# Performance work log

Hardware: AMD Instinct MI355X
Metric: run time of the kernel (lower is better)

The kernel has to match this reference:

```python
import jax, jax.numpy as jnp
import numpy as np

T, B, D = 512, 256, 2048   # seq_len, batch, input_dim
Q = 1                      # n_qubits == hidden_dim (forced by measure Linear(n_wires,1) applied to [B,1])
G = 4                      # gates: forget, input, update, output


def setup_inputs() -> dict:
    key = jax.random.key(0)
    ks = jax.random.split(key, 8)
    s_lin = 1.0 / np.sqrt(D + Q)   # torch Linear default init bound
    s_q = 1.0 / np.sqrt(Q)
    u = lambda k, shape, s: jax.random.uniform(k, shape, jnp.float32, -s, s)
    return {
        "inputs": jax.random.normal(ks[0], (T, B, D), jnp.float32),
        # stacked per-gate params (gate order: forget, input, update, output)
        "linear_w": u(ks[1], (G, Q, D + Q), s_lin),
        "linear_b": u(ks[2], (G, Q), s_lin),
        "enc_w": u(ks[3], (G, Q, Q), s_q),
        "enc_b": u(ks[4], (G, Q), s_q),
        "rx": jax.random.normal(ks[5], (G,), jnp.float32),   # rxs[0] per gate (only rxs[0] used in torch)
        "meas_w": u(ks[6], (G, 1, Q), s_q),
        "meas_b": u(ks[7], (G, 1), s_q),
    }


def reference(inputs, linear_w, linear_b, enc_w, enc_b, rx, meas_w, meas_b):
    b = inputs.shape[1]
    h0 = jnp.zeros((b, Q), inputs.dtype)
    c0 = jnp.zeros((b, Q), inputs.dtype)

    def step(carry, x):
        hx, cx = carry
        comb = jnp.concatenate([x, hx], axis=1)                      # [B, D+Q]
        # four classical linear gates, fused: [G, B, Q]
        pre = jnp.einsum('bd,gqd->gbq', comb, linear_w) + linear_b[:, None, :]
        # QGateLayer: encoder -> tanh(rxs[0] * angles summed over wires) -> measure
        ang = jnp.einsum('gbq,grq->gbr', pre, enc_w) + enc_b[:, None, :]
        s = jnp.tanh(jnp.sum(rx[:, None, None] * ang, axis=2, keepdims=True))  # [G, B, 1]
        vals = jnp.einsum('gbq,goq->gbo', s, meas_w) + meas_b[:, None, :]      # [G, B, 1]
        f = jax.nn.sigmoid(vals[0])
        i = jax.nn.sigmoid(vals[1])
        g = jnp.tanh(vals[2])
        o = jax.nn.sigmoid(vals[3])
        cx = f * cx + i * g
        hx = o * jnp.tanh(cx)
        return (hx, cx), hx

    (hx, cx), outs = jax.lax.scan(step, (h0, c0), inputs)
    return outs, hx, cx   # outs: [T, B, Q]
```

## Files before the change

kernel.cpp:

```cpp
#include <hip/hip_runtime.h>

#define TT 512
#define BB 256
#define DD 2048
#define DQ 2049
#define CH_T 128
#define CH_ROWS (CH_T * BB)
#define CH_WAVES (CH_ROWS / 16)
#define CH_BLOCKS (CH_WAVES / 4)

typedef float f32x4 __attribute__((ext_vector_type(4)));

__device__ __forceinline__ void ldg_nt(f32x4& d, const float* p) {
    asm volatile("global_load_dwordx4 %0, %1, off sc0 sc1 nt"
                 : "=v"(d) : "v"(p));
}
__device__ __forceinline__ void wait_vm4(f32x4& a, f32x4& b, f32x4& c, f32x4& d) {
    asm volatile("s_waitcnt vmcnt(4)" : "+v"(a), "+v"(b), "+v"(c), "+v"(d));
}
__device__ __forceinline__ void wait_vm0(f32x4& a, f32x4& b, f32x4& c, f32x4& d) {
    asm volatile("s_waitcnt vmcnt(0)" : "+v"(a), "+v"(b), "+v"(c), "+v"(d));
}

__device__ __forceinline__ float frcp(float x) { return __builtin_amdgcn_rcpf(x); }
__device__ __forceinline__ float ftanh(float x) {
    const float e = exp2f(x * 2.8853900817779268f);
    return 1.f - 2.f * frcp(1.f + e);
}
__device__ __forceinline__ float fsig(float x) {
    const float e = exp2f(-x * 1.4426950408889634f);
    return frcp(1.f + e);
}

__device__ __forceinline__ void gemm_part(
    const float* __restrict__ x, const float* __restrict__ lw,
    const float* __restrict__ lb, const float* __restrict__ ew,
    const float* __restrict__ ebv, const float* __restrict__ rx,
    f32x4* __restrict__ pre, int wave_base, int block_off)
{
    __shared__ f32x4 wlds[2048];
    float* wldsf = (float*)wlds;
    for (int j = threadIdx.x; j < 8192; j += 256) {
        const int it = j >> 10;
        const int g  = (j >> 8) & 3;
        wldsf[j] = lw[g * DQ + it * 256 + (j & 255)];
    }
    __syncthreads();

    const int lane = threadIdx.x & 63;
    const int wid  = wave_base + (blockIdx.x - block_off) * 4 + (threadIdx.x >> 6);
    const int row0 = wid * 16;

    float alv[4], bev[4], lbv[4];
#pragma unroll
    for (int g = 0; g < 4; ++g) {
        alv[g] = rx[g] * ew[g];
        bev[g] = rx[g] * ebv[g];
        lbv[g] = lb[g];
    }

    const float* xb = x + (size_t)row0 * DD + lane * 4;

    f32x4 xcur[4], xnx[4];
#pragma unroll
    for (int r = 0; r < 4; ++r) ldg_nt(xcur[r], xb + r * DD);

#pragma unroll
    for (int r0 = 0; r0 < 16; r0 += 4) {
        float a[4][4];
#pragma unroll
        for (int r = 0; r < 4; ++r)
#pragma unroll
            for (int g = 0; g < 4; ++g) a[r][g] = 0.f;

#pragma unroll
        for (int it = 0; it < 8; ++it) {
            const bool last = (it == 7) && (r0 == 12);
            if (!last) {
                const float* nb = (it < 7)
                    ? xb + (size_t)r0 * DD + (it + 1) * 256
                    : xb + (size_t)(r0 + 4) * DD;
#pragma unroll
                for (int r = 0; r < 4; ++r) ldg_nt(xnx[r], nb + r * DD);
            }
            if (last) wait_vm0(xcur[0], xcur[1], xcur[2], xcur[3]);
            else      wait_vm4(xcur[0], xcur[1], xcur[2], xcur[3]);

            const f32x4 w0 = wlds[(it * 4 + 0) * 64 + lane];
            const f32x4 w1 = wlds[(it * 4 + 1) * 64 + lane];
            const f32x4 w2 = wlds[(it * 4 + 2) * 64 + lane];
            const f32x4 w3 = wlds[(it * 4 + 3) * 64 + lane];
#pragma unroll
            for (int r = 0; r < 4; ++r) {
                const f32x4 xv = xcur[r];
                a[r][0] += xv[0] * w0[0] + xv[1] * w0[1] + xv[2] * w0[2] + xv[3] * w0[3];
                a[r][1] += xv[0] * w1[0] + xv[1] * w1[1] + xv[2] * w1[2] + xv[3] * w1[3];
                a[r][2] += xv[0] * w2[0] + xv[1] * w2[1] + xv[2] * w2[2] + xv[3] * w2[3];
                a[r][3] += xv[0] * w3[0] + xv[1] * w3[1] + xv[2] * w3[2] + xv[3] * w3[3];
            }
#pragma unroll
            for (int r = 0; r < 4; ++r) xcur[r] = xnx[r];
        }

#pragma unroll
        for (int s = 32; s >= 1; s >>= 1) {
#pragma unroll
            for (int r = 0; r < 4; ++r)
#pragma unroll
                for (int g = 0; g < 4; ++g)
                    a[r][g] += __shfl_xor(a[r][g], s);
        }
        if (lane == 0) {
#pragma unroll
            for (int r = 0; r < 4; ++r) {
                f32x4 o = {alv[0] * (a[r][0] + lbv[0]) + bev[0],
                           alv[1] * (a[r][1] + lbv[1]) + bev[1],
                           alv[2] * (a[r][2] + lbv[2]) + bev[2],
                           alv[3] * (a[r][3] + lbv[3]) + bev[3]};
                pre[row0 + r0 + r] = o;
            }
        }
    }
}

__device__ __forceinline__ void scan_part(
    const f32x4* __restrict__ pre, const float* __restrict__ lw,
    const float* __restrict__ ew, const float* __restrict__ ebv,
    const float* __restrict__ rx, const float* __restrict__ mw,
    const float* __restrict__ mb, float* __restrict__ out,
    float* __restrict__ hc, int t0)
{
    const int b = threadIdx.x;

    float aw[4], mww[4], mbb[4];
#pragma unroll
    for (int g = 0; g < 4; ++g) {
        aw[g]  = rx[g] * ew[g] * lw[g * DQ + DD];
        mww[g] = mw[g];
        mbb[g] = mb[g];
    }

    float h, c;
    if (t0 == 0) { h = 0.f; c = 0.f; }
    else         { h = hc[b]; c = hc[BB + b]; }

    f32x4 cur[8], nxt[8];
#pragma unroll
    for (int j = 0; j < 8; ++j) cur[j] = pre[(t0 + j) * BB + b];

    for (int tt = t0; tt < t0 + CH_T; tt += 8) {
        const int tn = tt + 8;
        if (tn < t0 + CH_T) {
#pragma unroll
            for (int j = 0; j < 8; ++j) nxt[j] = pre[(tn + j) * BB + b];
        }
#pragma unroll
        for (int j = 0; j < 8; ++j) {
            const f32x4 pc = cur[j];
            const float s0 = ftanh(fmaf(h, aw[0], pc[0]));
            const float s1 = ftanh(fmaf(h, aw[1], pc[1]));
            const float s2 = ftanh(fmaf(h, aw[2], pc[2]));
            const float s3 = ftanh(fmaf(h, aw[3], pc[3]));
            const float f  = fsig(fmaf(s0, mww[0], mbb[0]));
            const float i  = fsig(fmaf(s1, mww[1], mbb[1]));
            const float gg = ftanh(fmaf(s2, mww[2], mbb[2]));
            const float o  = fsig(fmaf(s3, mww[3], mbb[3]));
            c = f * c + i * gg;
            h = o * ftanh(c);
            out[(tt + j) * BB + b] = h;
        }
#pragma unroll
        for (int j = 0; j < 8; ++j) cur[j] = nxt[j];
    }

    hc[b]      = h;
    hc[BB + b] = c;
    if (t0 + CH_T == TT) {
        out[TT * BB + b]      = h;
        out[TT * BB + BB + b] = c;
    }
}

__global__ __launch_bounds__(256) void k_gemm0(
    const float* __restrict__ x, const float* __restrict__ lw,
    const float* __restrict__ lb, const float* __restrict__ ew,
    const float* __restrict__ ebv, const float* __restrict__ rx,
    f32x4* __restrict__ pre)
{
    gemm_part(x, lw, lb, ew, ebv, rx, pre, 0, 0);
}

__global__ __launch_bounds__(256) void k_mix(
    const float* __restrict__ x, const float* __restrict__ lw,
    const float* __restrict__ lb, const float* __restrict__ ew,
    const float* __restrict__ ebv, const float* __restrict__ rx,
    const float* __restrict__ mw, const float* __restrict__ mb,
    f32x4* __restrict__ pre, float* __restrict__ out,
    float* __restrict__ hc, int scan_t0, int wave_base)
{
    if (blockIdx.x == 0)
        scan_part(pre, lw, ew, ebv, rx, mw, mb, out, hc, scan_t0);
    else
        gemm_part(x, lw, lb, ew, ebv, rx, pre, wave_base, 1);
}

extern "C" void kernel_launch(void* const* d_in, const int* in_sizes, int n_in,
                              void* d_out, int out_size, void* d_ws, size_t ws_size,
                              hipStream_t stream) {
    const float* x   = (const float*)d_in[0];
    const float* lw  = (const float*)d_in[1];
    const float* lb  = (const float*)d_in[2];
    const float* ew  = (const float*)d_in[3];
    const float* ebv = (const float*)d_in[4];
    const float* rx  = (const float*)d_in[5];
    const float* mw  = (const float*)d_in[6];
    const float* mb  = (const float*)d_in[7];
    float* out = (float*)d_out;

    f32x4* pre = (f32x4*)d_ws;
    float* hc  = (float*)((char*)d_ws + (size_t)TT * BB * 16);

    k_gemm0<<<CH_BLOCKS, 256, 0, stream>>>(x, lw, lb, ew, ebv, rx, pre);
    k_mix<<<CH_BLOCKS + 1, 256, 0, stream>>>(x, lw, lb, ew, ebv, rx, mw, mb,
                                             pre, out, hc, 0, CH_WAVES);
    k_mix<<<CH_BLOCKS + 1, 256, 0, stream>>>(x, lw, lb, ew, ebv, rx, mw, mb,
                                             pre, out, hc, CH_T, 2 * CH_WAVES);
    k_mix<<<CH_BLOCKS + 1, 256, 0, stream>>>(x, lw, lb, ew, ebv, rx, mw, mb,
                                             pre, out, hc, 2 * CH_T, 3 * CH_WAVES);
    k_mix<<<1, 256, 0, stream>>>(x, lw, lb, ew, ebv, rx, mw, mb,
                                 pre, out, hc, 3 * CH_T, 0);
}
```

Before: 273.8 us.

## Halve rows per wave and deepen global-load prefetch to two stages

Each wave now handles 8 rows instead of 16, which doubles the number of GEMM blocks per chunk launch. The x loads move from a double buffer to a triple buffer, so two load groups stay in flight (vmcnt(8)). The goal is more memory-level parallelism and more waves in flight for this bandwidth-bound streaming GEMM. The cost is more blocks each reloading the 32KB weight tile into LDS and higher register pressure from the third buffer.

```diff
diff --git a/kernel.cpp b/kernel.cpp
--- a/kernel.cpp
+++ b/kernel.cpp
@@ -6,7 +6,8 @@
 #define DQ 2049
 #define CH_T 128
 #define CH_ROWS (CH_T * BB)
-#define CH_WAVES (CH_ROWS / 16)
+#define RPW 8
+#define CH_WAVES (CH_ROWS / RPW)
 #define CH_BLOCKS (CH_WAVES / 4)
 
 typedef float f32x4 __attribute__((ext_vector_type(4)));
@@ -14,6 +15,9 @@
 __device__ __forceinline__ void ldg_nt(f32x4& d, const float* p) {
     asm volatile("global_load_dwordx4 %0, %1, off sc0 sc1 nt"
                  : "=v"(d) : "v"(p));
+}
+__device__ __forceinline__ void wait_vm8(f32x4& a, f32x4& b, f32x4& c, f32x4& d) {
+    asm volatile("s_waitcnt vmcnt(8)" : "+v"(a), "+v"(b), "+v"(c), "+v"(d));
 }
 __device__ __forceinline__ void wait_vm4(f32x4& a, f32x4& b, f32x4& c, f32x4& d) {
     asm volatile("s_waitcnt vmcnt(4)" : "+v"(a), "+v"(b), "+v"(c), "+v"(d));
@@ -49,7 +53,7 @@
 
     const int lane = threadIdx.x & 63;
     const int wid  = wave_base + (blockIdx.x - block_off) * 4 + (threadIdx.x >> 6);
-    const int row0 = wid * 16;
+    const int row0 = wid * RPW;
 
     float alv[4], bev[4], lbv[4];
 #pragma unroll
@@ -59,65 +63,69 @@
         lbv[g] = lb[g];
     }
 
-    const float* xb = x + (size_t)row0 * DD + lane * 4;
-
-    f32x4 xcur[4], xnx[4];
-#pragma unroll
-    for (int r = 0; r < 4; ++r) ldg_nt(xcur[r], xb + r * DD);
-
-#pragma unroll
-    for (int r0 = 0; r0 < 16; r0 += 4) {
-        float a[4][4];
-#pragma unroll
-        for (int r = 0; r < 4; ++r)
-#pragma unroll
-            for (int g = 0; g < 4; ++g) a[r][g] = 0.f;
-
-#pragma unroll
-        for (int it = 0; it < 8; ++it) {
-            const bool last = (it == 7) && (r0 == 12);
-            if (!last) {
-                const float* nb = (it < 7)
-                    ? xb + (size_t)r0 * DD + (it + 1) * 256
-                    : xb + (size_t)(r0 + 4) * DD;
-#pragma unroll
-                for (int r = 0; r < 4; ++r) ldg_nt(xnx[r], nb + r * DD);
+    const float* xbp = x + (size_t)row0 * DD + lane * 4;
+
+    f32x4 xbuf[3][4];
+#pragma unroll
+    for (int r = 0; r < 4; ++r) ldg_nt(xbuf[0][r], xbp + (size_t)r * DD);
+#pragma unroll
+    for (int r = 0; r < 4; ++r) ldg_nt(xbuf[1][r], xbp + (size_t)r * DD + 256);
+
+    float a[4][4];
+#pragma unroll
+    for (int s = 0; s < 16; ++s) {
+        const int grp = s >> 3, it = s & 7;
+        if (it == 0) {
+#pragma unroll
+            for (int r = 0; r < 4; ++r)
+#pragma unroll
+                for (int q = 0; q < 4; ++q) a[r][q] = 0.f;
+        }
+        if (s + 2 < 16) {
+            const int s2 = s + 2, g2 = s2 >> 3, it2 = s2 & 7;
+#pragma unroll
+            for (int r = 0; r < 4; ++r)
+                ldg_nt(xbuf[s2 % 3][r],
+                       xbp + (size_t)(g2 * 4 + r) * DD + it2 * 256);
+        }
+        if (s < 14)
+            wait_vm8(xbuf[s % 3][0], xbuf[s % 3][1], xbuf[s % 3][2], xbuf[s % 3][3]);
+        else if (s == 14)
+            wait_vm4(xbuf[s % 3][0], xbuf[s % 3][1], xbuf[s % 3][2], xbuf[s % 3][3]);
+        else
+            wait_vm0(xbuf[s % 3][0], xbuf[s % 3][1], xbuf[s % 3][2], xbuf[s % 3][3]);
+
+        const f32x4 w0 = wlds[(it * 4 + 0) * 64 + lane];
+        const f32x4 w1 = wlds[(it * 4 + 1) * 64 + lane];
+        const f32x4 w2 = wlds[(it * 4 + 2) * 64 + lane];
+        const f32x4 w3 = wlds[(it * 4 + 3) * 64 + lane];
+#pragma unroll
+        for (int r = 0; r < 4; ++r) {
+            const f32x4 xv = xbuf[s % 3][r];
+            a[r][0] += xv[0] * w0[0] + xv[1] * w0[1] + xv[2] * w0[2] + xv[3] * w0[3];
+            a[r][1] += xv[0] * w1[0] + xv[1] * w1[1] + xv[2] * w1[2] + xv[3] * w1[3];
+            a[r][2] += xv[0] * w2[0] + xv[1] * w2[1] + xv[2] * w2[2] + xv[3] * w2[3];
+            a[r][3] += xv[0] * w3[0] + xv[1] * w3[1] + xv[2] * w3[2] + xv[3] * w3[3];
+        }
+
+        if (it == 7) {
+#pragma unroll
+            for (int st = 32; st >= 1; st >>= 1) {
+#pragma unroll
+                for (int r = 0; r < 4; ++r)
+#pragma unroll
+                    for (int q = 0; q < 4; ++q)
+                        a[r][q] += __shfl_xor(a[r][q], st);
             }
-            if (last) wait_vm0(xcur[0], xcur[1], xcur[2], xcur[3]);
-            else      wait_vm4(xcur[0], xcur[1], xcur[2], xcur[3]);
-
-            const f32x4 w0 = wlds[(it * 4 + 0) * 64 + lane];
-            const f32x4 w1 = wlds[(it * 4 + 1) * 64 + lane];
-            const f32x4 w2 = wlds[(it * 4 + 2) * 64 + lane];
-            const f32x4 w3 = wlds[(it * 4 + 3) * 64 + lane];
-#pragma unroll
-            for (int r = 0; r < 4; ++r) {
-                const f32x4 xv = xcur[r];
-                a[r][0] += xv[0] * w0[0] + xv[1] * w0[1] + xv[2] * w0[2] + xv[3] * w0[3];
-                a[r][1] += xv[0] * w1[0] + xv[1] * w1[1] + xv[2] * w1[2] + xv[3] * w1[3];
-                a[r][2] += xv[0] * w2[0] + xv[1] * w2[1] + xv[2] * w2[2] + xv[3] * w2[3];
-                a[r][3] += xv[0] * w3[0] + xv[1] * w3[1] + xv[2] * w3[2] + xv[3] * w3[3];
-            }
-#pragma unroll
-            for (int r = 0; r < 4; ++r) xcur[r] = xnx[r];
-        }
-
-#pragma unroll
-        for (int s = 32; s >= 1; s >>= 1) {
-#pragma unroll
-            for (int r = 0; r < 4; ++r)
-#pragma unroll
-                for (int g = 0; g < 4; ++g)
-                    a[r][g] += __shfl_xor(a[r][g], s);
-        }
-        if (lane == 0) {
-#pragma unroll
-            for (int r = 0; r < 4; ++r) {
-                f32x4 o = {alv[0] * (a[r][0] + lbv[0]) + bev[0],
-                           alv[1] * (a[r][1] + lbv[1]) + bev[1],
-                           alv[2] * (a[r][2] + lbv[2]) + bev[2],
-                           alv[3] * (a[r][3] + lbv[3]) + bev[3]};
-                pre[row0 + r0 + r] = o;
+            if (lane == 0) {
+#pragma unroll
+                for (int r = 0; r < 4; ++r) {
+                    f32x4 o = {alv[0] * (a[r][0] + lbv[0]) + bev[0],
+                               alv[1] * (a[r][1] + lbv[1]) + bev[1],
+                               alv[2] * (a[r][2] + lbv[2]) + bev[2],
+                               alv[3] * (a[r][3] + lbv[3]) + bev[3]};
+                    pre[row0 + grp * 4 + r] = o;
+                }
             }
         }
     }
```

Result: faster. 239.8 us, median of 2 (-12.4%).
